# Performance work log

Measured on AMD Instinct MI355X. Metric: run time of the kernel, lower is better.

The kernel has to match this reference:

```python
import jax, jax.numpy as jnp
import numpy as np

B, S, D, K = 8, 1024, 256, 16384


def setup_inputs() -> dict:
    key = jax.random.key(0)
    k1, k2 = jax.random.split(key)
    features = jax.random.normal(k1, (B, S, D), dtype=jnp.float32)
    centers = jax.random.normal(k2, (K, D), dtype=jnp.float32) * 0.1
    return {"features": features, "centers": centers}


def reference(features, centers):
    b, s, d = features.shape
    flat = features.reshape(-1, d)                      # (N, D)
    dist = (jnp.sum(flat * flat, axis=1, keepdims=True)
            - 2.0 * jnp.matmul(flat, centers.T)
            + jnp.sum(centers * centers, axis=1)[None, :])
    cluster_ids = jnp.argmin(dist, axis=-1)             # (N,)
    quantized = centers[cluster_ids].reshape(b, s, d)   # gather codebook rows
    return quantized, cluster_ids.reshape(b, s), dist
```

## Files before the change

### kernel.cpp

```cpp
#include <hip/hip_runtime.h>
#include <stdint.h>

#define N_ROWS 8192
#define D_DIM  256
#define K_CENT 16384

typedef __attribute__((ext_vector_type(8))) short bf16x8;
typedef __attribute__((ext_vector_type(4))) float f32x4;

__device__ __forceinline__ uint32_t fkey(float f) {
    uint32_t b = __float_as_uint(f);
    return (b & 0x80000000u) ? ~b : (b | 0x80000000u);
}

__device__ __forceinline__ unsigned short f2bf(float f) {
    uint32_t u = __float_as_uint(f);
    uint32_t r = u + 0x7FFFu + ((u >> 16) & 1u);
    return (unsigned short)(r >> 16);
}

__device__ __forceinline__ void gload_lds16(const void* g, void* l) {
    __builtin_amdgcn_global_load_lds(
        (const __attribute__((address_space(1))) void*)g,
        (__attribute__((address_space(3))) void*)l, 16, 0, 0);
}

__global__ __launch_bounds__(256)
void prep_kernel(const float* __restrict__ feat,
                 const float* __restrict__ cent,
                 unsigned short* __restrict__ Abf,
                 unsigned short* __restrict__ Bbf,
                 float* __restrict__ xnorm,
                 float* __restrict__ cnorm) {
    int gtid = blockIdx.x * blockDim.x + threadIdx.x;
    int wave = gtid >> 6;
    int lane = gtid & 63;
    if (wave >= N_ROWS + K_CENT) return;
    const float* src;
    unsigned short* dst;
    float* ndst;
    if (wave < N_ROWS) {
        src = feat + (size_t)wave * D_DIM;
        dst = Abf + (size_t)wave * D_DIM;
        ndst = xnorm + wave;
    } else {
        int r = wave - N_ROWS;
        src = cent + (size_t)r * D_DIM;
        dst = Bbf + (size_t)r * D_DIM;
        ndst = cnorm + r;
    }
    float4 v = ((const float4*)src)[lane];
    float s = v.x * v.x + v.y * v.y + v.z * v.z + v.w * v.w;
    ushort4 o;
    o.x = f2bf(v.x); o.y = f2bf(v.y); o.z = f2bf(v.z); o.w = f2bf(v.w);
    *(ushort4*)(dst + lane * 4) = o;
    #pragma unroll
    for (int off = 32; off >= 1; off >>= 1) s += __shfl_xor(s, off);
    if (lane == 0) *ndst = s;
}

#define GBM 128
#define GBN 128
#define GBK 32

__global__ __launch_bounds__(256, 2)
void dist_mfma(const unsigned short* __restrict__ Abf,
               const unsigned short* __restrict__ Bbf,
               const float* __restrict__ xnorm,
               const float* __restrict__ cnorm,
               float* __restrict__ dist,
               float* __restrict__ blockmins) {
    __shared__ unsigned short As[GBM][GBK];
    __shared__ unsigned short Bs[GBN][GBK];

    const int tid = threadIdx.x;
    const int lane = tid & 63;
    const int w = tid >> 6;
    const int wr = w >> 1, wc = w & 1;
    const int row0 = blockIdx.x * GBM;
    const int col0 = blockIdx.y * GBN;
    const int cl = lane & 15, kg = lane >> 4;

    f32x4 zero = {0.f, 0.f, 0.f, 0.f};
    f32x4 acc[4][4];
    #pragma unroll
    for (int m = 0; m < 4; ++m)
        #pragma unroll
        for (int n = 0; n < 4; ++n) acc[m][n] = zero;

    for (int kt = 0; kt < D_DIM / GBK; ++kt) {
        #pragma unroll
        for (int j = 0; j < 2; ++j) {
            int f = tid + 256 * j;
            int r = f >> 2, kq = f & 3;
            gload_lds16(Abf + (size_t)(row0 + r) * D_DIM + kt * GBK + kq * 8,
                        &As[0][0] + f * 8);
        }
        #pragma unroll
        for (int j = 0; j < 2; ++j) {
            int f = tid + 256 * j;
            int r = f >> 2, kq = f & 3;
            gload_lds16(Bbf + (size_t)(col0 + r) * D_DIM + kt * GBK + kq * 8,
                        &Bs[0][0] + f * 8);
        }
        __syncthreads();

        bf16x8 af[4], bfr[4];
        #pragma unroll
        for (int m = 0; m < 4; ++m)
            af[m] = *(const bf16x8*)&As[wr * 64 + m * 16 + cl][kg * 8];
        #pragma unroll
        for (int n = 0; n < 4; ++n)
            bfr[n] = *(const bf16x8*)&Bs[wc * 64 + n * 16 + cl][kg * 8];

        #pragma unroll
        for (int m = 0; m < 4; ++m)
            #pragma unroll
            for (int n = 0; n < 4; ++n)
                acc[m][n] = __builtin_amdgcn_mfma_f32_16x16x32_bf16(
                    bfr[n], af[m], acc[m][n], 0, 0, 0);
        __syncthreads();
    }

    const int bcol = blockIdx.y * 2 + wc;

    #pragma unroll
    for (int m = 0; m < 4; ++m) {
        const int row = row0 + wr * 64 + m * 16 + cl;
        const float xn = xnorm[row];
        float* drow = dist + (size_t)row * K_CENT;
        float rmin = 3.4e38f;
        #pragma unroll
        for (int n = 0; n < 4; ++n) {
            const int colb = col0 + wc * 64 + n * 16 + kg * 4;
            float4 cn4 = *(const float4*)&cnorm[colb];
            f32x4 a = acc[m][n];
            f32x4 d4;
            d4[0] = (xn - 2.f * a[0]) + cn4.x;
            d4[1] = (xn - 2.f * a[1]) + cn4.y;
            d4[2] = (xn - 2.f * a[2]) + cn4.z;
            d4[3] = (xn - 2.f * a[3]) + cn4.w;
            __builtin_nontemporal_store(d4, (f32x4*)(drow + colb));
            rmin = fminf(rmin,
                   fminf(fminf(d4[0], d4[1]), fminf(d4[2], d4[3])));
        }
        rmin = fminf(rmin, __shfl_xor(rmin, 16));
        rmin = fminf(rmin, __shfl_xor(rmin, 32));
        if (kg == 0)
            blockmins[(size_t)row * 256 + bcol] = rmin;
    }
}

__global__ __launch_bounds__(256)
void recheck_finalize(const float* __restrict__ feat,
                      const float* __restrict__ cent,
                      const float* __restrict__ xnorm,
                      const float* __restrict__ cnorm,
                      const float* __restrict__ blockmins,
                      const float* __restrict__ dist,
                      float* __restrict__ quant,
                      float* __restrict__ ids) {
    __shared__ float bms[4][256];
    const int tid = threadIdx.x;
    const int wv = tid >> 6;
    const int lane = tid & 63;
    const int row = blockIdx.x * 4 + wv;

    float4 xv = ((const float4*)(feat + (size_t)row * D_DIM))[lane];
    float4 bm4 = ((const float4*)(blockmins + (size_t)row * 256))[lane];
    ((float4*)&bms[wv][0])[lane] = bm4;

    float gmin = fminf(fminf(bm4.x, bm4.y), fminf(bm4.z, bm4.w));
    #pragma unroll
    for (int off = 32; off >= 1; off >>= 1)
        gmin = fminf(gmin, __shfl_xor(gmin, off));

    const float thr = gmin + 1.0f;
    const float xn = xnorm[row];
    const float* drow = dist + (size_t)row * K_CENT;

    unsigned long long best = 0xFFFFFFFFFFFFFFFFull;
    for (int b = 0; b < 256; ++b) {
        if (bms[wv][b] <= thr) {
            float d = drow[b * 64 + lane];
            unsigned long long m = __ballot(d <= thr);
            while (m) {
                int l = __ffsll((unsigned long long)m) - 1;
                m &= m - 1;
                int c = b * 64 + l;
                float4 cv = ((const float4*)(cent + (size_t)c * D_DIM))[lane];
                float p = fmaf(xv.x, cv.x,
                          fmaf(xv.y, cv.y,
                          fmaf(xv.z, cv.z, xv.w * cv.w)));
                #pragma unroll
                for (int off = 32; off >= 1; off >>= 1)
                    p += __shfl_xor(p, off);
                float dd = (xn - 2.f * p) + cnorm[c];
                unsigned long long key =
                    ((unsigned long long)fkey(dd) << 32) | (unsigned)c;
                best = (key < best) ? key : best;
            }
        }
    }
    const unsigned bidx = (unsigned)(best & 0xFFFFFFFFu);
    if (lane == 0) ids[row] = (float)bidx;
    float4 v = ((const float4*)(cent + (size_t)bidx * D_DIM))[lane];
    ((float4*)(quant + (size_t)row * D_DIM))[lane] = v;
}

extern "C" void kernel_launch(void* const* d_in, const int* in_sizes, int n_in,
                              void* d_out, int out_size, void* d_ws, size_t ws_size,
                              hipStream_t stream) {
    const float* feat = (const float*)d_in[0];
    const float* cent = (const float*)d_in[1];

    float* out = (float*)d_out;
    float* quant = out;
    float* ids   = out + 2097152;
    float* dist  = out + 2105344;

    char* ws = (char*)d_ws;
    unsigned short* Abf = (unsigned short*)ws;
    unsigned short* Bbf = (unsigned short*)(ws + (4u << 20));
    float* blockmins    = (float*)(ws + (12u << 20));
    float* xnorm        = (float*)(ws + (20u << 20));
    float* cnorm        = xnorm + N_ROWS;

    {
        int waves = N_ROWS + K_CENT;
        prep_kernel<<<(waves * 64 + 255) / 256, 256, 0, stream>>>(
            feat, cent, Abf, Bbf, xnorm, cnorm);
    }

    dist_mfma<<<dim3(N_ROWS / GBM, K_CENT / GBN), 256, 0, stream>>>(
        Abf, Bbf, xnorm, cnorm, dist, blockmins);

    recheck_finalize<<<N_ROWS / 4, 256, 0, stream>>>(
        feat, cent, xnorm, cnorm, blockmins, dist, quant, ids);
}
```

Baseline: 219.1 us.

## Stream centroid tiles through double-buffered LDS with register-resident feature rows

Replaces the 128x128 block-tiled GEMM with a streaming kernel. Each of 8 waves keeps its 16 feature rows in registers for the full D and walks 32 consecutive 64-column centroid tiles. The next tile is prefetched into a second LDS buffer while the current one is computed, and the epilogue writes dist and per-64-column block minima. The aim is to overlap global loads with MFMA and the large dist store traffic, and to drop repeated A-tile loads. The cost is lower arithmetic reuse per B tile (16 rows per wave), 64KB of LDS per block, and fewer blocks (512).

```diff
diff --git a/kernel.cpp b/kernel.cpp
--- a/kernel.cpp
+++ b/kernel.cpp
@@ -59,82 +59,79 @@
     if (lane == 0) *ndst = s;
 }
 
-#define GBM 128
-#define GBN 128
-#define GBK 32
-
-__global__ __launch_bounds__(256, 2)
-void dist_mfma(const unsigned short* __restrict__ Abf,
-               const unsigned short* __restrict__ Bbf,
-               const float* __restrict__ xnorm,
-               const float* __restrict__ cnorm,
-               float* __restrict__ dist,
-               float* __restrict__ blockmins) {
-    __shared__ unsigned short As[GBM][GBK];
-    __shared__ unsigned short Bs[GBN][GBK];
+#define TROWS 128
+#define TCOLS 64
+#define NT    32
+
+__global__ __launch_bounds__(512, 4)
+void dist_stream(const unsigned short* __restrict__ Abf,
+                 const unsigned short* __restrict__ Bbf,
+                 const float* __restrict__ xnorm,
+                 const float* __restrict__ cnorm,
+                 float* __restrict__ dist,
+                 float* __restrict__ blockmins) {
+    __shared__ unsigned short Bs[2][16384];
 
     const int tid = threadIdx.x;
     const int lane = tid & 63;
     const int w = tid >> 6;
-    const int wr = w >> 1, wc = w & 1;
-    const int row0 = blockIdx.x * GBM;
-    const int col0 = blockIdx.y * GBN;
     const int cl = lane & 15, kg = lane >> 4;
-
-    f32x4 zero = {0.f, 0.f, 0.f, 0.f};
-    f32x4 acc[4][4];
-    #pragma unroll
-    for (int m = 0; m < 4; ++m)
+    const int row0 = blockIdx.x * TROWS;
+    const int crange0 = blockIdx.y * (NT * TCOLS);
+
+    const int row = row0 + w * 16 + cl;
+    const float xn = xnorm[row];
+    float* const drow = dist + (size_t)row * K_CENT;
+
+    bf16x8 af[8];
+    #pragma unroll
+    for (int ks = 0; ks < 8; ++ks)
+        af[ks] = *(const bf16x8*)(Abf + (size_t)row * D_DIM + ks * 32 + kg * 8);
+
+    #pragma unroll
+    for (int j = 0; j < 4; ++j) {
+        int f = tid + 512 * j;
+        int ks = f >> 8, s = f & 255, r = s >> 2, kq = s & 3;
+        gload_lds16(Bbf + (size_t)(crange0 + r) * D_DIM + ks * 32 + kq * 8,
+                    &Bs[0][0] + f * 8);
+    }
+    __syncthreads();
+
+    int buf = 0;
+    for (int t = 0; t < NT; ++t) {
+        const int col0 = crange0 + t * TCOLS;
+
+        if (t + 1 < NT) {
+            #pragma unroll
+            for (int j = 0; j < 4; ++j) {
+                int f = tid + 512 * j;
+                int ks = f >> 8, s = f & 255, r = s >> 2, kq = s & 3;
+                gload_lds16(Bbf + (size_t)(col0 + TCOLS + r) * D_DIM + ks * 32 + kq * 8,
+                            &Bs[buf ^ 1][0] + f * 8);
+            }
+        }
+
+        f32x4 acc[4];
         #pragma unroll
-        for (int n = 0; n < 4; ++n) acc[m][n] = zero;
-
-    for (int kt = 0; kt < D_DIM / GBK; ++kt) {
+        for (int c = 0; c < 4; ++c) acc[c] = (f32x4){0.f, 0.f, 0.f, 0.f};
+
         #pragma unroll
-        for (int j = 0; j < 2; ++j) {
-            int f = tid + 256 * j;
-            int r = f >> 2, kq = f & 3;
-            gload_lds16(Abf + (size_t)(row0 + r) * D_DIM + kt * GBK + kq * 8,
-                        &As[0][0] + f * 8);
-        }
-        #pragma unroll
-        for (int j = 0; j < 2; ++j) {
-            int f = tid + 256 * j;
-            int r = f >> 2, kq = f & 3;
-            gload_lds16(Bbf + (size_t)(col0 + r) * D_DIM + kt * GBK + kq * 8,
-                        &Bs[0][0] + f * 8);
-        }
-        __syncthreads();
-
-        bf16x8 af[4], bfr[4];
-        #pragma unroll
-        for (int m = 0; m < 4; ++m)
-            af[m] = *(const bf16x8*)&As[wr * 64 + m * 16 + cl][kg * 8];
-        #pragma unroll
-        for (int n = 0; n < 4; ++n)
-            bfr[n] = *(const bf16x8*)&Bs[wc * 64 + n * 16 + cl][kg * 8];
-
-        #pragma unroll
-        for (int m = 0; m < 4; ++m)
+        for (int ks = 0; ks < 8; ++ks) {
             #pragma unroll
-            for (int n = 0; n < 4; ++n)
-                acc[m][n] = __builtin_amdgcn_mfma_f32_16x16x32_bf16(
-                    bfr[n], af[m], acc[m][n], 0, 0, 0);
-        __syncthreads();
-    }
-
-    const int bcol = blockIdx.y * 2 + wc;
-
-    #pragma unroll
-    for (int m = 0; m < 4; ++m) {
-        const int row = row0 + wr * 64 + m * 16 + cl;
-        const float xn = xnorm[row];
-        float* drow = dist + (size_t)row * K_CENT;
+            for (int c = 0; c < 4; ++c) {
+                bf16x8 b = *(const bf16x8*)
+                    &Bs[buf][ks * 2048 + (c * 16 + cl) * 32 + kg * 8];
+                acc[c] = __builtin_amdgcn_mfma_f32_16x16x32_bf16(
+                    b, af[ks], acc[c], 0, 0, 0);
+            }
+        }
+
         float rmin = 3.4e38f;
         #pragma unroll
-        for (int n = 0; n < 4; ++n) {
-            const int colb = col0 + wc * 64 + n * 16 + kg * 4;
+        for (int c = 0; c < 4; ++c) {
+            const int colb = col0 + c * 16 + kg * 4;
             float4 cn4 = *(const float4*)&cnorm[colb];
-            f32x4 a = acc[m][n];
+            f32x4 a = acc[c];
             f32x4 d4;
             d4[0] = (xn - 2.f * a[0]) + cn4.x;
             d4[1] = (xn - 2.f * a[1]) + cn4.y;
@@ -147,7 +144,10 @@
         rmin = fminf(rmin, __shfl_xor(rmin, 16));
         rmin = fminf(rmin, __shfl_xor(rmin, 32));
         if (kg == 0)
-            blockmins[(size_t)row * 256 + bcol] = rmin;
+            blockmins[(size_t)row * 256 + blockIdx.y * NT + t] = rmin;
+
+        __syncthreads();
+        buf ^= 1;
     }
 }
 
@@ -232,7 +232,7 @@
             feat, cent, Abf, Bbf, xnorm, cnorm);
     }
 
-    dist_mfma<<<dim3(N_ROWS / GBM, K_CENT / GBN), 256, 0, stream>>>(
+    dist_stream<<<dim3(N_ROWS / TROWS, 8), 512, 0, stream>>>(
         Abf, Bbf, xnorm, cnorm, dist, blockmins);
 
     recheck_finalize<<<N_ROWS / 4, 256, 0, stream>>>(
```

Result: slower. 254.9 us (+16.4%).
